# Kernel optimization log

Measured on AMD Instinct MI355X. Metric: run time of the kernel, lower is better.

Reference implementation:

```python
import jax, jax.numpy as jnp
import numpy as np

B, N, D_MEM, D_HID = 64, 65536, 1024, 1024


def setup_inputs() -> dict:
    key = jax.random.key(0)
    k1, k2, k3 = jax.random.split(key, 3)
    memory_bank = jax.random.normal(k1, (N, D_MEM), dtype=jnp.float32)
    decoder_state = jax.random.normal(k2, (B, D_HID), dtype=jnp.float32)
    # nn.Linear(memory_bank_size -> hidden_size, bias=False): weight [D_HID, D_MEM]
    W = jax.random.normal(k3, (D_HID, D_MEM), dtype=jnp.float32) / np.sqrt(D_MEM)
    # ragged tree sizes summing exactly to N (concrete, built on host)
    rng = np.random.default_rng(0)
    lens = rng.integers(512, 1536, size=B).astype(np.float64)
    lens = np.maximum(1, np.floor(lens * N / lens.sum()).astype(np.int64))
    lens[-1] += N - lens.sum()
    return {
        "memory_bank": memory_bank,
        "decoder_state": decoder_state,
        "W": W,
        "tree_node_num_lst": jnp.asarray(lens, dtype=jnp.int64),
    }


def reference(memory_bank, decoder_state, W, tree_node_num_lst):
    # segment id per node: tree index it belongs to (total_repeat_length keeps it jit-able)
    n_total = memory_bank.shape[0]
    batch = decoder_state.shape[0]
    seg = jnp.repeat(jnp.arange(batch), tree_node_num_lst, total_repeat_length=n_total)  # [N]
    # memory_project: one big GEMM instead of per-tree launches
    enc = memory_bank @ W.T                                  # [N, D_HID]
    # per-node score = <decoder_state[tree], enc[node]>
    scores = jnp.sum(enc * decoder_state[seg], axis=-1)      # [N]
    # segment (per-tree) stable softmax
    m = jax.ops.segment_max(scores, seg, num_segments=batch)  # [B]
    e = jnp.exp(scores - m[seg])                              # [N]
    z = jax.ops.segment_sum(e, seg, num_segments=batch)       # [B]
    attn = e / z[seg]                                         # [N]
    # context = attn-weighted sum of raw memory bank per tree
    context = jax.ops.segment_sum(attn[:, None] * memory_bank, seg, num_segments=batch)  # [B, D_MEM]
    return context
```

## Files before the change

### kernel.cpp

```cpp
#include <hip/hip_runtime.h>
#include <hip/hip_bf16.h>
#include <math.h>

#define B_TREES 64
#define N_NODES 65536
#define D 1024
#define D4 (D/4)

__global__ void offsets_kernel(const int* __restrict__ lens32, int* __restrict__ off) {
    if (threadIdx.x == 0 && blockIdx.x == 0) {
        long long s32 = 0;
        for (int b = 0; b < B_TREES; ++b) s32 += lens32[b];
        const bool is32 = (s32 == (long long)N_NODES);
        int acc = 0;
        off[0] = 0;
        for (int b = 0; b < B_TREES; ++b) {
            int len = is32 ? lens32[b] : (int)(((const long long*)lens32)[b]);
            acc += len;
            off[b + 1] = acc;
        }
    }
}

__global__ void v_kernel(const float* __restrict__ ds, const float* __restrict__ W,
                         float* __restrict__ v) {
    const int m  = blockIdx.x * 256 + threadIdx.x;
    const int b0 = blockIdx.y * 4;
    const int h0 = blockIdx.z * 128;
    float acc[4] = {0.f, 0.f, 0.f, 0.f};
    for (int h = h0; h < h0 + 128; ++h) {
        float wv = W[h * D + m];
        #pragma unroll
        for (int j = 0; j < 4; ++j)
            acc[j] += ds[(b0 + j) * D + h] * wv;
    }
    #pragma unroll
    for (int j = 0; j < 4; ++j)
        atomicAdd(&v[(b0 + j) * D + m], acc[j]);
}

__global__ void scores_kernel(const float4* __restrict__ mb, const float4* __restrict__ v,
                              const int* __restrict__ off, float* __restrict__ scores,
                              int* __restrict__ segarr) {
    const int wave = threadIdx.x >> 6;
    const int lane = threadIdx.x & 63;
    const int node = blockIdx.x * 4 + wave;

    int lo = 0, hi = B_TREES - 1;
    while (lo < hi) {
        int mid = (lo + hi + 1) >> 1;
        if (off[mid] <= node) lo = mid; else hi = mid - 1;
    }

    const float4* mrow = mb + (size_t)node * D4;
    const float4* vrow = v  + (size_t)lo   * D4;
    float acc = 0.f;
    #pragma unroll
    for (int k = 0; k < 4; ++k) {
        float4 a = mrow[k * 64 + lane];
        float4 c = vrow[k * 64 + lane];
        acc += a.x * c.x + a.y * c.y + a.z * c.z + a.w * c.w;
    }
    #pragma unroll
    for (int o = 32; o > 0; o >>= 1) acc += __shfl_down(acc, o, 64);
    if (lane == 0) {
        scores[node] = acc;
        segarr[node] = lo;
    }
}

__global__ void softmax_kernel(const int* __restrict__ off, float* __restrict__ scores) {
    const int b  = blockIdx.x;
    const int s0 = off[b], s1 = off[b + 1];
    const int tid = threadIdx.x;
    __shared__ float red[256];

    float mloc = -INFINITY;
    for (int i = s0 + tid; i < s1; i += 256) mloc = fmaxf(mloc, scores[i]);
    red[tid] = mloc; __syncthreads();
    for (int s = 128; s > 0; s >>= 1) {
        if (tid < s) red[tid] = fmaxf(red[tid], red[tid + s]);
        __syncthreads();
    }
    const float m = red[0]; __syncthreads();

    float zloc = 0.f;
    for (int i = s0 + tid; i < s1; i += 256) zloc += __expf(scores[i] - m);
    red[tid] = zloc; __syncthreads();
    for (int s = 128; s > 0; s >>= 1) {
        if (tid < s) red[tid] += red[tid + s];
        __syncthreads();
    }
    const float inv = 1.f / red[0]; __syncthreads();

    for (int i = s0 + tid; i < s1; i += 256)
        scores[i] = __expf(scores[i] - m) * inv;
}

__global__ void ctx_kernel(const float4* __restrict__ mb, const float* __restrict__ w,
                           const int* __restrict__ segarr, float* __restrict__ out) {
    const int n0 = blockIdx.x * 64;
    const int t  = threadIdx.x;
    float4 acc = make_float4(0.f, 0.f, 0.f, 0.f);
    int cur = segarr[n0];
    for (int i = 0; i < 64; ++i) {
        const int n = n0 + i;
        const int s = segarr[n];
        if (s != cur) {
            float* o = out + (size_t)cur * D + t * 4;
            atomicAdd(o + 0, acc.x); atomicAdd(o + 1, acc.y);
            atomicAdd(o + 2, acc.z); atomicAdd(o + 3, acc.w);
            acc = make_float4(0.f, 0.f, 0.f, 0.f);
            cur = s;
        }
        const float wv = w[n];
        const float4 m4 = mb[(size_t)n * D4 + t];
        acc.x += wv * m4.x; acc.y += wv * m4.y;
        acc.z += wv * m4.z; acc.w += wv * m4.w;
    }
    float* o = out + (size_t)cur * D + t * 4;
    atomicAdd(o + 0, acc.x); atomicAdd(o + 1, acc.y);
    atomicAdd(o + 2, acc.z); atomicAdd(o + 3, acc.w);
}

extern "C" void kernel_launch(void* const* d_in, const int* in_sizes, int n_in,
                              void* d_out, int out_size, void* d_ws, size_t ws_size,
                              hipStream_t stream) {
    const float* mb   = (const float*)d_in[0];
    const float* ds   = (const float*)d_in[1];
    const float* W    = (const float*)d_in[2];
    const int*   lens = (const int*)d_in[3];
    float*       out  = (float*)d_out;

    char* ws = (char*)d_ws;
    int*   off    = (int*)ws;
    float* v      = (float*)(ws + 512);
    float* scores = (float*)(ws + 512 + 64 * D * 4);
    int*   segarr = (int*)  (ws + 512 + 64 * D * 4 + N_NODES * 4);

    hipMemsetAsync(v, 0, 64 * D * sizeof(float), stream);
    hipMemsetAsync(out, 0, B_TREES * D * sizeof(float), stream);

    offsets_kernel<<<1, 64, 0, stream>>>(lens, off);

    {
        dim3 grid(4, 16, 8);
        v_kernel<<<grid, 256, 0, stream>>>(ds, W, v);
    }

    scores_kernel<<<N_NODES / 4, 256, 0, stream>>>(
        (const float4*)mb, (const float4*)v, off, scores, segarr);

    softmax_kernel<<<B_TREES, 256, 0, stream>>>(off, scores);

    ctx_kernel<<<N_NODES / 64, 256, 0, stream>>>(
        (const float4*)mb, scores, segarr, out);
}
```

Measured before the change: 436.4 us.

## Fuse scores, segment softmax and context into single-pass online-softmax kernel

Splits each tree into fixed-size node pieces and has one wave per piece compute scores, a running max/sum and a rescaled weighted context in one pass over the memory bank. A finalize kernel merges the per-piece partial results per tree. This removes the second full read of the memory bank, the separate softmax kernel and the atomic accumulation. The cost is a serial per-node loop inside each wave with fewer waves in flight, plus writing and re-reading per-piece context partials.

```diff
diff --git a/kernel.cpp b/kernel.cpp
--- a/kernel.cpp
+++ b/kernel.cpp
@@ -6,19 +6,39 @@
 #define N_NODES 65536
 #define D 1024
 #define D4 (D/4)
+#define PIECE 16
+#define MAXP (N_NODES/PIECE + B_TREES)
 
-__global__ void offsets_kernel(const int* __restrict__ lens32, int* __restrict__ off) {
+__global__ void setup_kernel(const int* __restrict__ lens32,
+                             int* __restrict__ off, int* __restrict__ pbase) {
     if (threadIdx.x == 0 && blockIdx.x == 0) {
         long long s32 = 0;
         for (int b = 0; b < B_TREES; ++b) s32 += lens32[b];
         const bool is32 = (s32 == (long long)N_NODES);
-        int acc = 0;
-        off[0] = 0;
+        int acc = 0, pacc = 0;
+        off[0] = 0; pbase[0] = 0;
         for (int b = 0; b < B_TREES; ++b) {
             int len = is32 ? lens32[b] : (int)(((const long long*)lens32)[b]);
-            acc += len;
-            off[b + 1] = acc;
+            acc  += len;
+            pacc += (len + PIECE - 1) / PIECE;
+            off[b + 1]   = acc;
+            pbase[b + 1] = pacc;
         }
+    }
+}
+
+__global__ void pieces_kernel(const int* __restrict__ off, const int* __restrict__ pbase,
+                              int* __restrict__ pseg, int* __restrict__ pstart,
+                              int* __restrict__ plen) {
+    const int b  = blockIdx.x;
+    const int s0 = off[b], s1 = off[b + 1];
+    const int np = pbase[b + 1] - pbase[b];
+    for (int i = threadIdx.x; i < np; i += blockDim.x) {
+        int st = s0 + i * PIECE;
+        int p  = pbase[b] + i;
+        pseg[p]   = b;
+        pstart[p] = st;
+        plen[p]   = min(PIECE, s1 - st);
     }
 }
 
@@ -39,88 +59,80 @@
         atomicAdd(&v[(b0 + j) * D + m], acc[j]);
 }
 
-__global__ void scores_kernel(const float4* __restrict__ mb, const float4* __restrict__ v,
-                              const int* __restrict__ off, float* __restrict__ scores,
-                              int* __restrict__ segarr) {
+__global__ __launch_bounds__(256) void fused_kernel(
+        const float4* __restrict__ mb, const float4* __restrict__ v,
+        const int* __restrict__ pseg, const int* __restrict__ pstart,
+        const int* __restrict__ plen, const int* __restrict__ pbase,
+        float* __restrict__ pm, float* __restrict__ pz, float4* __restrict__ pctx) {
     const int wave = threadIdx.x >> 6;
     const int lane = threadIdx.x & 63;
-    const int node = blockIdx.x * 4 + wave;
+    const int p    = blockIdx.x * 4 + wave;
+    if (p >= pbase[B_TREES]) return;
 
-    int lo = 0, hi = B_TREES - 1;
-    while (lo < hi) {
-        int mid = (lo + hi + 1) >> 1;
-        if (off[mid] <= node) lo = mid; else hi = mid - 1;
+    const int seg = pseg[p];
+    const int s0  = pstart[p];
+    const int ln  = plen[p];
+
+    const float4* vrow = v + (size_t)seg * D4;
+    const float4 v0 = vrow[lane], v1 = vrow[64 + lane],
+                 v2 = vrow[128 + lane], v3 = vrow[192 + lane];
+
+    float4 a0 = make_float4(0.f,0.f,0.f,0.f), a1 = a0, a2 = a0, a3 = a0;
+    float rm = -INFINITY, rz = 0.f;
+
+    for (int i = 0; i < ln; ++i) {
+        const float4* mrow = mb + (size_t)(s0 + i) * D4;
+        const float4 m0 = mrow[lane],       m1 = mrow[64 + lane],
+                     m2 = mrow[128 + lane], m3 = mrow[192 + lane];
+        float d0 = m0.x*v0.x + m0.y*v0.y + m0.z*v0.z + m0.w*v0.w;
+        float d1 = m1.x*v1.x + m1.y*v1.y + m1.z*v1.z + m1.w*v1.w;
+        float d2 = m2.x*v2.x + m2.y*v2.y + m2.z*v2.z + m2.w*v2.w;
+        float d3 = m3.x*v3.x + m3.y*v3.y + m3.z*v3.z + m3.w*v3.w;
+        float d  = (d0 + d1) + (d2 + d3);
+        #pragma unroll
+        for (int o = 32; o > 0; o >>= 1) d += __shfl_xor(d, o, 64);
+
+        const float nm = fmaxf(rm, d);
+        const float sc = __expf(rm - nm);
+        const float w  = __expf(d - nm);
+        a0.x = a0.x*sc + w*m0.x; a0.y = a0.y*sc + w*m0.y;
+        a0.z = a0.z*sc + w*m0.z; a0.w = a0.w*sc + w*m0.w;
+        a1.x = a1.x*sc + w*m1.x; a1.y = a1.y*sc + w*m1.y;
+        a1.z = a1.z*sc + w*m1.z; a1.w = a1.w*sc + w*m1.w;
+        a2.x = a2.x*sc + w*m2.x; a2.y = a2.y*sc + w*m2.y;
+        a2.z = a2.z*sc + w*m2.z; a2.w = a2.w*sc + w*m2.w;
+        a3.x = a3.x*sc + w*m3.x; a3.y = a3.y*sc + w*m3.y;
+        a3.z = a3.z*sc + w*m3.z; a3.w = a3.w*sc + w*m3.w;
+        rz = rz*sc + w;
+        rm = nm;
     }
 
-    const float4* mrow = mb + (size_t)node * D4;
-    const float4* vrow = v  + (size_t)lo   * D4;
-    float acc = 0.f;
-    #pragma unroll
-    for (int k = 0; k < 4; ++k) {
-        float4 a = mrow[k * 64 + lane];
-        float4 c = vrow[k * 64 + lane];
-        acc += a.x * c.x + a.y * c.y + a.z * c.z + a.w * c.w;
-    }
-    #pragma unroll
-    for (int o = 32; o > 0; o >>= 1) acc += __shfl_down(acc, o, 64);
-    if (lane == 0) {
-        scores[node] = acc;
-        segarr[node] = lo;
-    }
+    if (lane == 0) { pm[p] = rm; pz[p] = rz; }
+    float4* o = pctx + (size_t)p * D4;
+    o[lane] = a0; o[64 + lane] = a1; o[128 + lane] = a2; o[192 + lane] = a3;
 }
 
-__global__ void softmax_kernel(const int* __restrict__ off, float* __restrict__ scores) {
+__global__ void finalize_kernel(const int* __restrict__ pbase,
+                                const float* __restrict__ pm, const float* __restrict__ pz,
+                                const float4* __restrict__ pctx, float4* __restrict__ out) {
     const int b  = blockIdx.x;
-    const int s0 = off[b], s1 = off[b + 1];
-    const int tid = threadIdx.x;
-    __shared__ float red[256];
+    const int t  = threadIdx.x;
+    const int q0 = pbase[b], q1 = pbase[b + 1];
 
-    float mloc = -INFINITY;
-    for (int i = s0 + tid; i < s1; i += 256) mloc = fmaxf(mloc, scores[i]);
-    red[tid] = mloc; __syncthreads();
-    for (int s = 128; s > 0; s >>= 1) {
-        if (tid < s) red[tid] = fmaxf(red[tid], red[tid + s]);
-        __syncthreads();
+    float mb_ = -INFINITY;
+    for (int q = q0; q < q1; ++q) mb_ = fmaxf(mb_, pm[q]);
+    float zb = 0.f;
+    for (int q = q0; q < q1; ++q) zb += pz[q] * __expf(pm[q] - mb_);
+    const float inv = 1.f / zb;
+
+    float4 acc = make_float4(0.f,0.f,0.f,0.f);
+    for (int q = q0; q < q1; ++q) {
+        const float s = __expf(pm[q] - mb_);
+        const float4 c = pctx[(size_t)q * D4 + t];
+        acc.x += s * c.x; acc.y += s * c.y; acc.z += s * c.z; acc.w += s * c.w;
     }
-    const float m = red[0]; __syncthreads();
-
-    float zloc = 0.f;
-    for (int i = s0 + tid; i < s1; i += 256) zloc += __expf(scores[i] - m);
-    red[tid] = zloc; __syncthreads();
-    for (int s = 128; s > 0; s >>= 1) {
-        if (tid < s) red[tid] += red[tid + s];
-        __syncthreads();
-    }
-    const float inv = 1.f / red[0]; __syncthreads();
-
-    for (int i = s0 + tid; i < s1; i += 256)
-        scores[i] = __expf(scores[i] - m) * inv;
-}
-
-__global__ void ctx_kernel(const float4* __restrict__ mb, const float* __restrict__ w,
-                           const int* __restrict__ segarr, float* __restrict__ out) {
-    const int n0 = blockIdx.x * 64;
-    const int t  = threadIdx.x;
-    float4 acc = make_float4(0.f, 0.f, 0.f, 0.f);
-    int cur = segarr[n0];
-    for (int i = 0; i < 64; ++i) {
-        const int n = n0 + i;
-        const int s = segarr[n];
-        if (s != cur) {
-            float* o = out + (size_t)cur * D + t * 4;
-            atomicAdd(o + 0, acc.x); atomicAdd(o + 1, acc.y);
-            atomicAdd(o + 2, acc.z); atomicAdd(o + 3, acc.w);
-            acc = make_float4(0.f, 0.f, 0.f, 0.f);
-            cur = s;
-        }
-        const float wv = w[n];
-        const float4 m4 = mb[(size_t)n * D4 + t];
-        acc.x += wv * m4.x; acc.y += wv * m4.y;
-        acc.z += wv * m4.z; acc.w += wv * m4.w;
-    }
-    float* o = out + (size_t)cur * D + t * 4;
-    atomicAdd(o + 0, acc.x); atomicAdd(o + 1, acc.y);
-    atomicAdd(o + 2, acc.z); atomicAdd(o + 3, acc.w);
+    acc.x *= inv; acc.y *= inv; acc.z *= inv; acc.w *= inv;
+    out[(size_t)b * D4 + t] = acc;
 }
 
 extern "C" void kernel_launch(void* const* d_in, const int* in_sizes, int n_in,
@@ -133,26 +145,30 @@
     float*       out  = (float*)d_out;
 
     char* ws = (char*)d_ws;
-    int*   off    = (int*)ws;
-    float* v      = (float*)(ws + 512);
-    float* scores = (float*)(ws + 512 + 64 * D * 4);
-    int*   segarr = (int*)  (ws + 512 + 64 * D * 4 + N_NODES * 4);
+    int*   off    = (int*)(ws + 0);
+    int*   pbase  = (int*)(ws + 512);
+    float* v      = (float*)(ws + 1024);
+    int*   pseg   = (int*)(ws + 1024 + 262144);
+    int*   pstart = (int*)(ws + 1024 + 262144 + 32768);
+    int*   plen   = (int*)(ws + 1024 + 262144 + 65536);
+    float* pm     = (float*)(ws + 1024 + 262144 + 98304);
+    float* pz     = (float*)(ws + 1024 + 262144 + 131072);
+    float4* pctx  = (float4*)(ws + 1024 + 262144 + 163840);
 
     hipMemsetAsync(v, 0, 64 * D * sizeof(float), stream);
-    hipMemsetAsync(out, 0, B_TREES * D * sizeof(float), stream);
 
-    offsets_kernel<<<1, 64, 0, stream>>>(lens, off);
+    setup_kernel<<<1, 64, 0, stream>>>(lens, off, pbase);
+    pieces_kernel<<<B_TREES, 256, 0, stream>>>(off, pbase, pseg, pstart, plen);
 
     {
         dim3 grid(4, 16, 8);
         v_kernel<<<grid, 256, 0, stream>>>(ds, W, v);
     }
 
-    scores_kernel<<<N_NODES / 4, 256, 0, stream>>>(
-        (const float4*)mb, (const float4*)v, off, scores, segarr);
+    fused_kernel<<<(MAXP + 3) / 4, 256, 0, stream>>>(
+        (const float4*)mb, (const float4*)v, pseg, pstart, plen, pbase,
+        pm, pz, pctx);
 
-    softmax_kernel<<<B_TREES, 256, 0, stream>>>(off, scores);
-
-    ctx_kernel<<<N_NODES / 64, 256, 0, stream>>>(
-        (const float4*)mb, scores, segarr, out);
+    finalize_kernel<<<B_TREES, 256, 0, stream>>>(
+        pbase, pm, pz, pctx, (float4*)out);
 }
```

New measurement: 442.0 us. Within noise of the previous version (+1.3%).
